# Kernel optimization log

Measured on AMD Instinct MI355X. Metric: run time of the kernel, lower is better.

The kernel has to match this reference:

```python
import jax, jax.numpy as jnp
import numpy as np

MAX_PATCH = 8   # max_patch_size: fixed span length
D_MODEL = 128
VOCAB = 256     # byte vocabulary
B, T = 16, 16384


def setup_inputs() -> dict:
    key = jax.random.key(0)
    k1, k2 = jax.random.split(key)
    x_u8 = jax.random.randint(k1, (B, T), 0, VOCAB, dtype=jnp.int32)
    byte_embed = jax.random.normal(k2, (VOCAB, D_MODEL), dtype=jnp.float32)
    return {"x_u8": x_u8, "byte_embed": byte_embed}


def reference(x_u8, byte_embed):
    # heuristic='fixed': spans are contiguous chunks of MAX_PATCH bytes.
    # Per span: embedding lookup then mean over the span -> [B, Tp, D].
    b, t = x_u8.shape
    tp = t // MAX_PATCH  # T divisible by MAX_PATCH (no ragged tail)
    emb = byte_embed[x_u8]  # gather: [B, T, D]
    out = emb.reshape(b, tp, MAX_PATCH, D_MODEL).mean(axis=2)  # [B, Tp, D]
    return out
```

## Files before the change

kernel.cpp:

```cpp
#include <hip/hip_runtime.h>
#include <hip/hip_bf16.h>


__global__ __launch_bounds__(256) void blt_patch_mean_kernel(
    const int* __restrict__ x,
    const float4* __restrict__ emb4,
    float4* __restrict__ out4,
    int n4)
{
    int g = blockIdx.x * blockDim.x + threadIdx.x;
    if (g >= n4) return;

    int patch = g >> 5;
    int col   = g & 31;

    const int* idx = x + patch * 8;
    int4 i0 = *reinterpret_cast<const int4*>(idx);
    int4 i1 = *reinterpret_cast<const int4*>(idx + 4);

    float4 acc = make_float4(0.f, 0.f, 0.f, 0.f);
    #define ACCUM(r) { float4 v = emb4[(r) * 32 + col];                       \
                       acc.x += v.x; acc.y += v.y; acc.z += v.z; acc.w += v.w; }
    ACCUM(i0.x); ACCUM(i0.y); ACCUM(i0.z); ACCUM(i0.w);
    ACCUM(i1.x); ACCUM(i1.y); ACCUM(i1.z); ACCUM(i1.w);
    #undef ACCUM

    const float s = 0.125f;
    acc.x *= s; acc.y *= s; acc.z *= s; acc.w *= s;
    out4[g] = acc;
}

extern "C" void kernel_launch(void* const* d_in, const int* in_sizes, int n_in,
                              void* d_out, int out_size, void* d_ws, size_t ws_size,
                              hipStream_t stream)
{
    const int*    x    = (const int*)d_in[0];
    const float4* emb4 = (const float4*)d_in[1];
    float4*       out4 = (float4*)d_out;

    int n4 = out_size / 4;
    int block = 256;
    int grid = (n4 + block - 1) / block;
    blt_patch_mean_kernel<<<grid, block, 0, stream>>>(x, emb4, out4, n4);
}
```

Before: 13.22 us.

## Stage embedding table in LDS with persistent grid-stride blocks

```diff
diff --git a/kernel.cpp b/kernel.cpp
--- a/kernel.cpp
+++ b/kernel.cpp
@@ -2,44 +2,56 @@
 #include <hip/hip_bf16.h>
 
 
-__global__ __launch_bounds__(256) void blt_patch_mean_kernel(
-    const int* __restrict__ x,
+#define NPATCH  32768
+#define TPB     1024
+#define NBLK    256
+#define NGROUPS ((NBLK * TPB) / 32)
+#define ITERS   (NPATCH / NGROUPS)
+
+__global__ __launch_bounds__(TPB, 1) void blt_patch_mean_lds(
+    const int4* __restrict__ x4,
     const float4* __restrict__ emb4,
-    float4* __restrict__ out4,
-    int n4)
+    float4* __restrict__ out4)
 {
-    int g = blockIdx.x * blockDim.x + threadIdx.x;
-    if (g >= n4) return;
+    extern __shared__ float4 tbl[];
 
-    int patch = g >> 5;
-    int col   = g & 31;
+    #pragma unroll
+    for (int i = 0; i < 8; ++i) {
+        int k = i * TPB + threadIdx.x;
+        tbl[k] = emb4[k];
+    }
+    __syncthreads();
 
-    const int* idx = x + patch * 8;
-    int4 i0 = *reinterpret_cast<const int4*>(idx);
-    int4 i1 = *reinterpret_cast<const int4*>(idx + 4);
+    const int group0 = ((int)blockIdx.x * TPB + (int)threadIdx.x) >> 5;
+    const int col    = threadIdx.x & 31;
 
-    float4 acc = make_float4(0.f, 0.f, 0.f, 0.f);
-    #define ACCUM(r) { float4 v = emb4[(r) * 32 + col];                       \
-                       acc.x += v.x; acc.y += v.y; acc.z += v.z; acc.w += v.w; }
-    ACCUM(i0.x); ACCUM(i0.y); ACCUM(i0.z); ACCUM(i0.w);
-    ACCUM(i1.x); ACCUM(i1.y); ACCUM(i1.z); ACCUM(i1.w);
-    #undef ACCUM
+    #pragma unroll
+    for (int it = 0; it < ITERS; ++it) {
+        const int p = group0 + it * NGROUPS;
 
-    const float s = 0.125f;
-    acc.x *= s; acc.y *= s; acc.z *= s; acc.w *= s;
-    out4[g] = acc;
+        int4 i0 = x4[p * 2];
+        int4 i1 = x4[p * 2 + 1];
+
+        float4 acc = make_float4(0.f, 0.f, 0.f, 0.f);
+        #define ACCUM(r) { float4 v = tbl[(r) * 32 + col];                     \
+                           acc.x += v.x; acc.y += v.y; acc.z += v.z; acc.w += v.w; }
+        ACCUM(i0.x); ACCUM(i0.y); ACCUM(i0.z); ACCUM(i0.w);
+        ACCUM(i1.x); ACCUM(i1.y); ACCUM(i1.z); ACCUM(i1.w);
+        #undef ACCUM
+
+        const float s = 0.125f;
+        acc.x *= s; acc.y *= s; acc.z *= s; acc.w *= s;
+        out4[p * 32 + col] = acc;
+    }
 }
 
 extern "C" void kernel_launch(void* const* d_in, const int* in_sizes, int n_in,
                               void* d_out, int out_size, void* d_ws, size_t ws_size,
                               hipStream_t stream)
 {
-    const int*    x    = (const int*)d_in[0];
+    const int4*   x4   = (const int4*)d_in[0];
     const float4* emb4 = (const float4*)d_in[1];
     float4*       out4 = (float4*)d_out;
 
-    int n4 = out_size / 4;
-    int block = 256;
-    int grid = (n4 + block - 1) / block;
-    blt_patch_mean_kernel<<<grid, block, 0, stream>>>(x, emb4, out4, n4);
+    blt_patch_mean_lds<<<NBLK, TPB, 131072, stream>>>(x4, emb4, out4);
 }
```

New measurement: 11.67 us. -11.7%, faster.
